# Kernel tuning notes

Hardware: AMD Instinct MI355X
Metric: run time of the kernel (lower is better)

The kernel has to match this reference:

```python
import jax, jax.numpy as jnp
import numpy as np

B, L, H, N, NL = 2, 160000, 128, 64, 4
TS, MR, CLS, LMAX = 1001, 16, 88, 1024
REP = TS * MR  # 16016


def setup_inputs() -> dict:
    key = jax.random.key(0)
    ks = jax.random.split(key, 16)
    def g(k, shape, s=0.02):
        return jax.random.normal(k, shape, jnp.float32) * s
    return {
        "x": jax.random.normal(ks[0], (B, L), jnp.float32),
        "enc_w": g(ks[1], (1, H), 1.0),
        "enc_b": g(ks[2], (H,)),
        "log_dt": jax.random.uniform(ks[3], (NL, H), jnp.float32, float(np.log(1e-3)), float(np.log(1e-1))),
        "log_A_real": jnp.log(0.5 * jnp.ones((NL, H, N), jnp.float32)),
        "A_imag": jnp.tile((np.pi * np.arange(N, dtype=np.float32))[None, None, :], (NL, H, 1)),
        "C_re": g(ks[4], (NL, H, N), 0.5 ** 0.5),
        "C_im": g(ks[5], (NL, H, N), 0.5 ** 0.5),
        "D": g(ks[6], (NL, H), 1.0),
        "out_w": g(ks[7], (NL, 2 * H, H), H ** -0.5),
        "out_b": g(ks[8], (NL, 2 * H)),
        "ln_g": jnp.ones((NL, H), jnp.float32),
        "ln_b": jnp.zeros((NL, H), jnp.float32),
        "dec_w": g(ks[9], (H, REP), H ** -0.5),
        "dec_b": g(ks[10], (REP,)),
        "head_w": g(ks[11], (4, MR, CLS), MR ** -0.5),
        "head_b": g(ks[12], (4, CLS)),
    }


def _s4_layer(u, log_dt, log_A_real, A_imag, C_re, C_im, D, out_w, out_b):
    # u: (B, H, L). S4D-style diagonal SSM kernel of length LMAX + FFT causal conv.
    dt = jnp.exp(log_dt)                         # (H,)
    A = -jnp.exp(log_A_real) + 1j * A_imag       # (H, N)
    C = C_re + 1j * C_im                         # (H, N)
    dtA = A * dt[:, None]                        # (H, N)
    Ct = C * (jnp.exp(dtA) - 1.0) / A            # ZOH-ish discretization
    l = jnp.arange(LMAX)
    vand = jnp.exp(dtA[:, :, None] * l)          # (H, N, LMAX) Vandermonde
    K = 2.0 * jnp.real(jnp.einsum('hn,hnl->hl', Ct, vand))  # (H, LMAX)
    n = L + LMAX                                 # linear (causal) conv via FFT
    uf = jnp.fft.rfft(u, n=n)                    # (B, H, n//2+1)
    kf = jnp.fft.rfft(K, n=n)                    # (H, n//2+1)
    y = jnp.fft.irfft(uf * kf[None], n=n)[..., :L]
    y = y + D[None, :, None] * u                 # skip connection
    y = jax.nn.gelu(y)
    # position-wise output linear H -> 2H, then GLU
    z = jnp.einsum('bhl,ph->bpl', y, out_w) + out_b[None, :, None]
    a, b = jnp.split(z, 2, axis=1)
    return a * jax.nn.sigmoid(b)


def _layernorm(v, g, b):
    # v: (B, L, H), normalize over H
    mu = v.mean(-1, keepdims=True)
    var = v.var(-1, keepdims=True)
    return (v - mu) / jnp.sqrt(var + 1e-5) * g + b


def reference(x, enc_w, enc_b, log_dt, log_A_real, A_imag, C_re, C_im, D,
              out_w, out_b, ln_g, ln_b, dec_w, dec_b, head_w, head_b):
    # encoder: (B, L, 1) -> (B, L, H)
    h = x[..., None] * enc_w[0][None, None, :] + enc_b  # (B, L, H)
    u = jnp.swapaxes(h, 1, 2)                            # (B, H, L)
    for i in range(NL):
        z = _s4_layer(u, log_dt[i], log_A_real[i], A_imag[i], C_re[i], C_im[i],
                      D[i], out_w[i], out_b[i])
        u = z + u                                        # residual
        v = _layernorm(jnp.swapaxes(u, 1, 2), ln_g[i], ln_b[i])  # post-norm
        u = jnp.swapaxes(v, 1, 2)
    feat = jnp.swapaxes(u, 1, 2).mean(axis=1)            # (B, H) mean-pool over L
    rep = feat @ dec_w + dec_b                           # (B, REP)
    rep = rep.reshape(B, TS, MR)                         # (B, 1001, 16)
    # 4 heads: [reg_onset, reg_offset, frame, velocity] stacked -> (4, B, TS, CLS)
    outs = jnp.einsum('btm,kmc->kbtc', rep, head_w) + head_b[:, None, None, :]
    return outs
```

## Files before the change

### kernel.cpp

```cpp
#include <hip/hip_runtime.h>
#include <math.h>

#define B_ 2
#define L_ 160000
#define H_ 128
#define N_ 64
#define NL_ 4
#define LMAX_ 1024
#define TS_ 1001
#define MR_ 16
#define CLS_ 88
#define REP_ 16016

#define NSUB_ 79
#define NJ_ 40
#define WIN_ 3208
#define WINS_ 3216
#define OUTB_ 2048
#define KE_STRIDE_ 1536
#define NST_ 10

typedef unsigned short ushort_t;
typedef unsigned int uint_t;
typedef short bf16x8 __attribute__((ext_vector_type(8)));
typedef float f32x4 __attribute__((ext_vector_type(4)));

__device__ __forceinline__ float bf2f(ushort_t h) {
  uint_t u = ((uint_t)h) << 16;
  return __uint_as_float(u);
}
__device__ __forceinline__ ushort_t f2bf(float f) {
  uint_t u = __float_as_uint(f);
  uint_t r = (u + 0x7fffu + ((u >> 16) & 1u)) >> 16;
  return (ushort_t)r;
}

__device__ __forceinline__ void lds_barrier() {
  asm volatile("s_waitcnt lgkmcnt(0)" ::: "memory");
  __builtin_amdgcn_sched_barrier(0);
  __builtin_amdgcn_s_barrier();
  __builtin_amdgcn_sched_barrier(0);
}

__global__ __launch_bounds__(256) void k_encode(const float* __restrict__ x,
                                                const float* __restrict__ enc_w,
                                                const float* __restrict__ enc_b,
                                                ushort_t* __restrict__ u) {
  int idx = blockIdx.x * 256 + threadIdx.x;
  int idx8 = idx * 8;
  int b = idx8 / (H_ * L_);
  int rem = idx8 - b * (H_ * L_);
  int h = rem / L_;
  int l = rem - h * L_;
  float w = enc_w[h], bb = enc_b[h];
  float4 x0 = *(const float4*)(x + b * L_ + l);
  float4 x1 = *(const float4*)(x + b * L_ + l + 4);
  union { ushort_t s[8]; uint4 v; } o;
  o.s[0] = f2bf(x0.x * w + bb); o.s[1] = f2bf(x0.y * w + bb);
  o.s[2] = f2bf(x0.z * w + bb); o.s[3] = f2bf(x0.w * w + bb);
  o.s[4] = f2bf(x1.x * w + bb); o.s[5] = f2bf(x1.y * w + bb);
  o.s[6] = f2bf(x1.z * w + bb); o.s[7] = f2bf(x1.w * w + bb);
  *(uint4*)(u + (size_t)(b * H_ + h) * L_ + l) = o.v;
}

__global__ __launch_bounds__(256) void k_ct(const float* __restrict__ log_dt,
                                            const float* __restrict__ log_A_real,
                                            const float* __restrict__ A_imag,
                                            const float* __restrict__ C_re,
                                            const float* __restrict__ C_im,
                                            float* __restrict__ ct,
                                            float* __restrict__ feat) {
  int idx = blockIdx.x * 256 + threadIdx.x;
  if (idx < B_ * H_) feat[idx] = 0.f;
  if (idx >= NL_ * H_ * N_) return;
  int h = (idx / N_) % H_;
  int i = idx / (N_ * H_);
  float dt = expf(log_dt[i * H_ + h]);
  float are = -expf(log_A_real[idx]);
  float aim = A_imag[idx];
  float dr = are * dt, di = aim * dt;
  float e = expf(dr);
  float si, co;
  sincosf(di, &si, &co);
  float er = e * co - 1.0f;
  float ei = e * si;
  float den = are * are + aim * aim;
  float qr = (er * are + ei * aim) / den;
  float qi = (ei * are - er * aim) / den;
  float cr = C_re[idx], cim = C_im[idx];
  double dd = (double)aim * (double)dt * 0.15915494309189535;
  dd -= floor(dd);
  uint_t P = (uint_t)(unsigned long long)(dd * 4294967296.0);
  ct[idx * 4 + 0] = dr;
  ct[idx * 4 + 1] = __uint_as_float(P);
  ct[idx * 4 + 2] = cr * qr - cim * qi;
  ct[idx * 4 + 3] = cr * qi + cim * qr;
}

__global__ __launch_bounds__(256) void k_ke(const float* __restrict__ ct,
                                            ushort_t* __restrict__ Ke) {
  int q = blockIdx.x & 3;
  int ih = blockIdx.x >> 2;
  __shared__ float4 cs[N_];
  if (threadIdx.x < N_) cs[threadIdx.x] = ((const float4*)ct)[ih * N_ + threadIdx.x];
  __syncthreads();
  for (int s = q * 384 + threadIdx.x; s < (q + 1) * 384; s += 256) {
    int d = s - 256;
    float val = 0.f;
    if (d >= 0 && d < LMAX_) {
      float fl = (float)d;
      float acc = 0.f;
      #pragma unroll 4
      for (int n = 0; n < N_; n++) {
        float4 qv = cs[n];
        float e = __expf(qv.x * fl);
        uint_t ph = __float_as_uint(qv.y) * (uint_t)d;
        float ang = (float)ph * 2.3283064365386963e-10f;
        float si = __builtin_amdgcn_sinf(ang);
        float co = __builtin_amdgcn_cosf(ang);
        acc += e * (qv.z * co - qv.w * si);
      }
      val = 2.f * acc;
    }
    Ke[(size_t)ih * KE_STRIDE_ + s] = f2bf(val);
  }
}

__global__ __launch_bounds__(256) void k_wprep(const float* __restrict__ W,
                                               ushort_t* __restrict__ Wb) {
  int idx = blockIdx.x * 256 + threadIdx.x;
  Wb[idx] = f2bf(W[idx]);
}

__global__ __launch_bounds__(256) void k_conv_mfma(const ushort_t* __restrict__ u,
                                                   const ushort_t* __restrict__ Ke,
                                                   const float* __restrict__ Dv,
                                                   ushort_t* __restrict__ y,
                                                   int layer) {
  int sub = blockIdx.x % NSUB_;
  int bh = blockIdx.x / NSUB_;
  int h = bh & (H_ - 1);
  int O0 = sub * OUTB_;
  int Gmax = O0 + 2063;
  __shared__ ushort_t win[4 * WINS_];
  __shared__ ushort_t kes[KE_STRIDE_];
  int tid = threadIdx.x;
  int lane = tid & 63, w = tid >> 6;
  int m = lane & 15, g = lane >> 4;

  {
    const ushort_t* keh0 = Ke + (size_t)(layer * H_ + h) * KE_STRIDE_;
    if (tid < KE_STRIDE_ / 8)
      *(bf16x8*)(kes + 8 * tid) = *(const bf16x8*)(keh0 + 8 * tid);
  }

  const ushort_t* ubh = u + (size_t)bh * L_;
  for (int T = tid; T < WIN_ / 8; T += 256) {
    int topt = Gmax - 8 * T;
    ushort_t vb[16];
    if (topt - 15 >= 0 && topt < L_) {
      union { uint4 q[2]; ushort_t s[16]; } ld;
      ld.q[0] = *(const uint4*)(ubh + topt - 15);
      ld.q[1] = *(const uint4*)(ubh + topt - 7);
      #pragma unroll
      for (int d = 0; d < 16; d++) vb[d] = ld.s[15 - d];
    } else {
      #pragma unroll
      for (int d = 0; d < 16; d++) {
        int gl = topt - d;
        vb[d] = (gl >= 0 && gl < L_) ? ubh[gl] : (ushort_t)0;
      }
    }
    #pragma unroll
    for (int p = 0; p < 4; p++) {
      union { bf16x8 v; ushort_t s[8]; } gr;
      #pragma unroll
      for (int e = 0; e < 8; e++) gr.s[e] = vb[p + e];
      *(bf16x8*)((char*)win + p * (2 * WINS_) + 16 * T) = gr.v;
    }
  }
  lds_barrier();

  const char* wb = (const char*)win;
  const ushort_t* kf0 = kes + 16 * m + 8 * g;
  int l0A = O0 + (w << 9);
  f32x4 accA = {0.f, 0.f, 0.f, 0.f}, accB = {0.f, 0.f, 0.f, 0.f};
  int t0 = Gmax - l0A - m + 8 * g - 256;
  bf16x8 ring[8];
  #pragma unroll
  for (int s = -8; s < NJ_; s++) {
    int tS = t0 + (s << 5);
    int pS = tS & 3;
    const char* base = wb + pS * (2 * WINS_) + 2 * (tS - pS);
    union { bf16x8 v; short4 h[2]; } f;
    f.h[0] = *(const short4*)base;
    f.h[1] = *(const short4*)(base + 8);
    if (s >= 0)
      accA = __builtin_amdgcn_mfma_f32_16x16x32_bf16(f.v, ring[s & 7], accA, 0, 0, 0);
    if (s <= 31) {
      bf16x8 kn = *(const bf16x8*)(kf0 + 32 * (s + 8));
      accB = __builtin_amdgcn_mfma_f32_16x16x32_bf16(f.v, kn, accB, 0, 0, 0);
      ring[(s + 8) & 7] = kn;
    }
  }

  float Dh = Dv[layer * H_ + h];
  ushort_t* ybh = y + (size_t)bh * L_;
  #pragma unroll
  for (int tile = 0; tile < 2; tile++) {
    f32x4 acc = tile ? accB : accA;
    int l0 = l0A + tile * 256;
    int outb = l0 + 16 * m + 4 * g;
    int tu = Gmax - outb - 3;
    int pu = tu & 3;
    union { short4 s4; ushort_t us[4]; } uu;
    uu.s4 = *(const short4*)(wb + pu * (2 * WINS_) + 2 * (tu - pu));
    union { ushort_t s[4]; short4 v; } pk;
    #pragma unroll
    for (int r = 0; r < 4; r++) {
      float uval = bf2f(uu.us[3 - r]);
      float v = acc[r] + Dh * uval;
      float z2 = 1.5957691216057308f * (v + 0.044715f * v * v * v);
      pk.s[r] = f2bf(v / (1.f + __expf(-z2)));
    }
    if (outb < L_) *(short4*)(ybh + outb) = pk.v;
  }
}

__global__ __launch_bounds__(256) void k_fused(const ushort_t* __restrict__ y,
                                               const ushort_t* __restrict__ Wb,
                                               const float* __restrict__ ob,
                                               ushort_t* __restrict__ u,
                                               const float* __restrict__ lng,
                                               const float* __restrict__ lnb,
                                               int last,
                                               float* __restrict__ feat) {
  __shared__ ushort_t yT[64 * 136];
  __shared__ float redS[4 * 64] __attribute__((aligned(16)));
  __shared__ float redQ[4 * 64] __attribute__((aligned(16)));
  __shared__ float redM[64] __attribute__((aligned(16)));
  __shared__ float redR[64] __attribute__((aligned(16)));
  int lblk = blockIdx.x, b = blockIdx.y;
  int tid = threadIdx.x;
  int lane = tid & 63, w = tid >> 6;
  int m = lane & 15, g = lane >> 4;
  int s = tid & 7, kkb = tid >> 3;
  int Lbase = lblk * (NST_ * 64);

  bf16x8 Wf[4][4];
  #pragma unroll
  for (int pj = 0; pj < 4; pj++) {
    int pbase = (pj < 2) ? (32 * w + 16 * pj) : (128 + 32 * w + 16 * (pj - 2));
    const ushort_t* wrow = Wb + (pbase + m) * 128 + 8 * g;
    #pragma unroll
    for (int ks = 0; ks < 4; ks++)
      Wf[pj][ks] = *(const bf16x8*)(wrow + 32 * ks);
  }
  float oba[2], obs[2], gam[2], bet[2];
  #pragma unroll
  for (int pj = 0; pj < 2; pj++) {
    int pa = 32 * w + 16 * pj + m;
    oba[pj] = ob[pa];
    obs[pj] = ob[pa + 128];
    gam[pj] = lng[pa];
    bet[pj] = lnb[pa];
  }

  uint4 sr[4];
  short4 un[2][4];
  #pragma unroll
  for (int p = 0; p < 4; p++)
    sr[p] = *(const uint4*)(y + ((size_t)b * H_ + kkb + 32 * p) * L_ + Lbase + 8 * s);
  #pragma unroll
  for (int pj = 0; pj < 2; pj++) {
    int pa = 32 * w + 16 * pj + m;
    const ushort_t* urow = u + (size_t)(b * H_ + pa) * L_ + Lbase;
    #pragma unroll
    for (int lj = 0; lj < 4; lj++)
      un[pj][lj] = *(const short4*)(urow + 16 * lj + 4 * g);
  }

  float poolAcc[2] = {0.f, 0.f};

  #pragma unroll
  for (int st = 0; st < NST_; st++) {
    int lc0 = Lbase + st * 64;

    uint4 srn[4];
    short4 unn[2][4];
    if (st < NST_ - 1) {
      int lc1 = lc0 + 64;
      #pragma unroll
      for (int p = 0; p < 4; p++)
        srn[p] = *(const uint4*)(y + ((size_t)b * H_ + kkb + 32 * p) * L_ + lc1 + 8 * s);
      #pragma unroll
      for (int pj = 0; pj < 2; pj++) {
        int pa = 32 * w + 16 * pj + m;
        const ushort_t* urow = u + (size_t)(b * H_ + pa) * L_ + lc1;
        #pragma unroll
        for (int lj = 0; lj < 4; lj++)
          unn[pj][lj] = *(const short4*)(urow + 16 * lj + 4 * g);
      }
    }

    #pragma unroll
    for (int p = 0; p < 4; p++) {
      int kk = kkb + 32 * p;
      const ushort_t* hp = (const ushort_t*)&sr[p];
      int sw = 8 * ((kk >> 3) ^ s) + (kk & 7);
      #pragma unroll
      for (int e = 0; e < 8; e++)
        yT[(8 * s + e) * 136 + sw] = hp[e];
    }
    lds_barrier();

    f32x4 acc[4][4];
    #pragma unroll
    for (int pj = 0; pj < 4; pj++)
      #pragma unroll
      for (int lj = 0; lj < 4; lj++) acc[pj][lj] = (f32x4){0.f, 0.f, 0.f, 0.f};
    #pragma unroll
    for (int ks = 0; ks < 4; ks++) {
      bf16x8 yf[4];
      #pragma unroll
      for (int lj = 0; lj < 4; lj++) {
        int l = 16 * lj + m;
        yf[lj] = *(const bf16x8*)(yT + l * 136 + 8 * ((4 * ks + g) ^ (l >> 3)));
      }
      #pragma unroll
      for (int pj = 0; pj < 4; pj++)
        #pragma unroll
        for (int lj = 0; lj < 4; lj++)
          acc[pj][lj] = __builtin_amdgcn_mfma_f32_16x16x32_bf16(yf[lj], Wf[pj][ks],
                                                                acc[pj][lj], 0, 0, 0);
    }

    #pragma unroll
    for (int pj = 0; pj < 2; pj++) {
      #pragma unroll
      for (int lj = 0; lj < 4; lj++) {
        #pragma unroll
        for (int r = 0; r < 4; r++) {
          float a = acc[pj][lj][r] + oba[pj];
          float sv = acc[pj + 2][lj][r] + obs[pj];
          float uor = bf2f(((const ushort_t*)&un[pj][lj])[r]);
          acc[pj][lj][r] = a * (1.f / (1.f + __expf(-sv))) + uor;
        }
      }
    }

    #pragma unroll
    for (int lj = 0; lj < 4; lj++) {
      #pragma unroll
      for (int r = 0; r < 4; r++) {
        float v0 = acc[0][lj][r], v1 = acc[1][lj][r];
        float sm = v0 + v1, q = v0 * v0 + v1 * v1;
        sm += __shfl_xor(sm, 1);  q += __shfl_xor(q, 1);
        sm += __shfl_xor(sm, 2);  q += __shfl_xor(q, 2);
        sm += __shfl_xor(sm, 4);  q += __shfl_xor(q, 4);
        sm += __shfl_xor(sm, 8);  q += __shfl_xor(q, 8);
        if (m == 0) {
          int l = 16 * lj + 4 * g + r;
          redS[w * 64 + l] = sm;
          redQ[w * 64 + l] = q;
        }
      }
    }
    lds_barrier();
    if (tid < 64) {
      float sm = redS[tid] + redS[64 + tid] + redS[128 + tid] + redS[192 + tid];
      float q = redQ[tid] + redQ[64 + tid] + redQ[128 + tid] + redQ[192 + tid];
      float mean = sm * (1.f / 128.f);
      float var = q * (1.f / 128.f) - mean * mean;
      redM[tid] = mean;
      redR[tid] = rsqrtf(var + 1e-5f);
    }
    lds_barrier();

    #pragma unroll
    for (int pj = 0; pj < 2; pj++) {
      int pa = 32 * w + 16 * pj + m;
      ushort_t* urow = u + (size_t)(b * H_ + pa) * L_ + lc0;
      #pragma unroll
      for (int lj = 0; lj < 4; lj++) {
        int l0 = 16 * lj + 4 * g;
        f32x4 mn = *(const f32x4*)(redM + l0);
        f32x4 rs = *(const f32x4*)(redR + l0);
        if (!last) {
          union { ushort_t sx[4]; short4 v; } pk;
          #pragma unroll
          for (int r = 0; r < 4; r++)
            pk.sx[r] = f2bf((acc[pj][lj][r] - mn[r]) * rs[r] * gam[pj] + bet[pj]);
          *(short4*)(urow + l0) = pk.v;
        } else {
          #pragma unroll
          for (int r = 0; r < 4; r++)
            poolAcc[pj] += (acc[pj][lj][r] - mn[r]) * rs[r] * gam[pj] + bet[pj];
        }
      }
    }

    #pragma unroll
    for (int p = 0; p < 4; p++) sr[p] = srn[p];
    #pragma unroll
    for (int pj = 0; pj < 2; pj++)
      #pragma unroll
      for (int lj = 0; lj < 4; lj++) un[pj][lj] = unn[pj][lj];
  }

  if (last) {
    #pragma unroll
    for (int pj = 0; pj < 2; pj++) {
      int pa = 32 * w + 16 * pj + m;
      float pool = poolAcc[pj];
      pool += __shfl_xor(pool, 16);
      pool += __shfl_xor(pool, 32);
      if (g == 0) atomicAdd(&feat[b * H_ + pa], pool * (1.f / L_));
    }
  }
}

__global__ __launch_bounds__(256) void k_dec(const float* __restrict__ feat,
                                             const float* __restrict__ dw,
                                             const float* __restrict__ db,
                                             float* __restrict__ rep) {
  int idx = blockIdx.x * 256 + threadIdx.x;
  if (idx >= B_ * REP_) return;
  int b = idx / REP_, r = idx - b * REP_;
  float s = db[r];
  #pragma unroll 8
  for (int h = 0; h < H_; h++) s = fmaf(feat[b * H_ + h], dw[h * REP_ + r], s);
  rep[idx] = s;
}

__global__ __launch_bounds__(256) void k_head(const float* __restrict__ rep,
                                              const float* __restrict__ hw,
                                              const float* __restrict__ hb,
                                              float* __restrict__ out) {
  int idx = blockIdx.x * 256 + threadIdx.x;
  if (idx >= 4 * B_ * TS_ * CLS_) return;
  int c = idx % CLS_;
  int t = (idx / CLS_) % TS_;
  int b = (idx / (CLS_ * TS_)) % B_;
  int k = idx / (CLS_ * TS_ * B_);
  float s = hb[k * CLS_ + c];
  const float* rp = rep + ((long long)b * TS_ + t) * MR_;
  #pragma unroll
  for (int m = 0; m < MR_; m++) s = fmaf(rp[m], hw[(k * MR_ + m) * CLS_ + c], s);
  out[idx] = s;
}

extern "C" void kernel_launch(void* const* d_in, const int* in_sizes, int n_in,
                              void* d_out, int out_size, void* d_ws, size_t ws_size,
                              hipStream_t stream) {
  const float* x = (const float*)d_in[0];
  const float* enc_w = (const float*)d_in[1];
  const float* enc_b = (const float*)d_in[2];
  const float* log_dt = (const float*)d_in[3];
  const float* log_A_real = (const float*)d_in[4];
  const float* A_imag = (const float*)d_in[5];
  const float* C_re = (const float*)d_in[6];
  const float* C_im = (const float*)d_in[7];
  const float* Dv = (const float*)d_in[8];
  const float* out_w = (const float*)d_in[9];
  const float* out_b = (const float*)d_in[10];
  const float* ln_g = (const float*)d_in[11];
  const float* ln_b = (const float*)d_in[12];
  const float* dec_w = (const float*)d_in[13];
  const float* dec_b = (const float*)d_in[14];
  const float* head_w = (const float*)d_in[15];
  const float* head_b = (const float*)d_in[16];

  if (ws_size < 167000000ULL) return;

  float* ws = (float*)d_ws;
  ushort_t* u = (ushort_t*)ws;
  ushort_t* y = (ushort_t*)(ws + 20480000);
  ushort_t* Ke = (ushort_t*)(ws + 20480000 + 20480000);
  float* ct = ws + 20480000 + 20480000 + 393216;
  ushort_t* Wb = (ushort_t*)(ct + 131072);
  float* feat = ct + 131072 + 65536;
  float* rep = feat + 256;

  k_encode<<<(B_ * H_ * L_ / 8 + 255) / 256, 256, 0, stream>>>(x, enc_w, enc_b, u);
  k_ct<<<(NL_ * H_ * N_ + 255) / 256, 256, 0, stream>>>(log_dt, log_A_real, A_imag,
                                                        C_re, C_im, ct, feat);
  k_ke<<<NL_ * H_ * 4, 256, 0, stream>>>(ct, Ke);
  k_wprep<<<NL_ * 256 * 128 / 256, 256, 0, stream>>>(out_w, Wb);

  for (int i = 0; i < NL_; i++) {
    k_conv_mfma<<<B_ * H_ * NSUB_, 256, 0, stream>>>(u, Ke, Dv, y, i);
    k_fused<<<dim3(L_ / (NST_ * 64), B_), 256, 0, stream>>>(
        y, Wb + (size_t)i * 256 * 128, out_b + i * 256, u,
        ln_g + i * H_, ln_b + i * H_, (i == NL_ - 1) ? 1 : 0, feat);
  }
  k_dec<<<(B_ * REP_ + 255) / 256, 256, 0, stream>>>(feat, dec_w, dec_b, rep);
  k_head<<<(4 * B_ * TS_ * CLS_ + 255) / 256, 256, 0, stream>>>(rep, head_w, head_b,
                                                               (float*)d_out);
}
```

Before: 994.7 us.

## Store activations in blocked (B, L/64, H, 64) layout to contiguize fused-kernel tiles

```diff
diff --git a/kernel.cpp b/kernel.cpp
--- a/kernel.cpp
+++ b/kernel.cpp
@@ -12,13 +12,15 @@
 #define CLS_ 88
 #define REP_ 16016
 
+#define NB_ 2500
+#define HB_ 8192
 #define NSUB_ 79
 #define NJ_ 40
 #define WIN_ 3208
 #define WINS_ 3216
 #define OUTB_ 2048
 #define KE_STRIDE_ 1536
-#define NST_ 10
+#define NSTF_ 4
 
 typedef unsigned short ushort_t;
 typedef unsigned int uint_t;
@@ -60,7 +62,8 @@
   o.s[2] = f2bf(x0.z * w + bb); o.s[3] = f2bf(x0.w * w + bb);
   o.s[4] = f2bf(x1.x * w + bb); o.s[5] = f2bf(x1.y * w + bb);
   o.s[6] = f2bf(x1.z * w + bb); o.s[7] = f2bf(x1.w * w + bb);
-  *(uint4*)(u + (size_t)(b * H_ + h) * L_ + l) = o.v;
+  size_t addr = ((size_t)b * NB_ + (l >> 6)) * HB_ + h * 64 + (l & 63);
+  *(uint4*)(u + addr) = o.v;
 }
 
 __global__ __launch_bounds__(256) void k_ct(const float* __restrict__ log_dt,
@@ -140,6 +143,7 @@
   int sub = blockIdx.x % NSUB_;
   int bh = blockIdx.x / NSUB_;
   int h = bh & (H_ - 1);
+  int b = bh >> 7;
   int O0 = sub * OUTB_;
   int Gmax = O0 + 2063;
   __shared__ ushort_t win[4 * WINS_];
@@ -154,23 +158,28 @@
       *(bf16x8*)(kes + 8 * tid) = *(const bf16x8*)(keh0 + 8 * tid);
   }
 
-  const ushort_t* ubh = u + (size_t)bh * L_;
+  const ushort_t* UB = u + (size_t)b * NB_ * HB_ + h * 64;
   for (int T = tid; T < WIN_ / 8; T += 256) {
     int topt = Gmax - 8 * T;
+    ushort_t tmp[16];
+    #pragma unroll
+    for (int half = 0; half < 2; half++) {
+      int x = topt - 15 + 8 * half;
+      if (x >= 0 && x + 7 < L_) {
+        *(uint4*)&tmp[8 * half] =
+            *(const uint4*)(UB + (size_t)(x >> 6) * HB_ + (x & 63));
+      } else {
+        #pragma unroll
+        for (int j = 0; j < 8; j++) {
+          int gl = x + j;
+          tmp[8 * half + j] = (gl >= 0 && gl < L_)
+              ? UB[(size_t)(gl >> 6) * HB_ + (gl & 63)] : (ushort_t)0;
+        }
+      }
+    }
     ushort_t vb[16];
-    if (topt - 15 >= 0 && topt < L_) {
-      union { uint4 q[2]; ushort_t s[16]; } ld;
-      ld.q[0] = *(const uint4*)(ubh + topt - 15);
-      ld.q[1] = *(const uint4*)(ubh + topt - 7);
-      #pragma unroll
-      for (int d = 0; d < 16; d++) vb[d] = ld.s[15 - d];
-    } else {
-      #pragma unroll
-      for (int d = 0; d < 16; d++) {
-        int gl = topt - d;
-        vb[d] = (gl >= 0 && gl < L_) ? ubh[gl] : (ushort_t)0;
-      }
-    }
+    #pragma unroll
+    for (int d = 0; d < 16; d++) vb[d] = tmp[15 - d];
     #pragma unroll
     for (int p = 0; p < 4; p++) {
       union { bf16x8 v; ushort_t s[8]; } gr;
@@ -205,7 +214,7 @@
   }
 
   float Dh = Dv[layer * H_ + h];
-  ushort_t* ybh = y + (size_t)bh * L_;
+  ushort_t* YB = y + (size_t)b * NB_ * HB_ + h * 64;
   #pragma unroll
   for (int tile = 0; tile < 2; tile++) {
     f32x4 acc = tile ? accB : accA;
@@ -223,7 +232,8 @@
       float z2 = 1.5957691216057308f * (v + 0.044715f * v * v * v);
       pk.s[r] = f2bf(v / (1.f + __expf(-z2)));
     }
-    if (outb < L_) *(short4*)(ybh + outb) = pk.v;
+    if (outb < L_)
+      *(short4*)(YB + (size_t)(outb >> 6) * HB_ + (outb & 63)) = pk.v;
   }
 }
 
@@ -245,7 +255,7 @@
   int lane = tid & 63, w = tid >> 6;
   int m = lane & 15, g = lane >> 4;
   int s = tid & 7, kkb = tid >> 3;
-  int Lbase = lblk * (NST_ * 64);
+  int nb0 = lblk * NSTF_;
 
   bf16x8 Wf[4][4];
   #pragma unroll
@@ -266,40 +276,46 @@
     bet[pj] = lnb[pa];
   }
 
+  const ushort_t* ybase = y + (size_t)b * NB_ * HB_;
+  ushort_t* ubase = u + (size_t)b * NB_ * HB_;
+
   uint4 sr[4];
   short4 un[2][4];
+  {
+    const ushort_t* yb = ybase + (size_t)nb0 * HB_;
+    #pragma unroll
+    for (int p = 0; p < 4; p++)
+      sr[p] = *(const uint4*)(yb + (kkb + 32 * p) * 64 + 8 * s);
+    const ushort_t* ub = ubase + (size_t)nb0 * HB_;
+    #pragma unroll
+    for (int pj = 0; pj < 2; pj++) {
+      int pa = 32 * w + 16 * pj + m;
+      #pragma unroll
+      for (int lj = 0; lj < 4; lj++)
+        un[pj][lj] = *(const short4*)(ub + pa * 64 + 16 * lj + 4 * g);
+    }
+  }
+
+  float poolAcc[2] = {0.f, 0.f};
+
   #pragma unroll
-  for (int p = 0; p < 4; p++)
-    sr[p] = *(const uint4*)(y + ((size_t)b * H_ + kkb + 32 * p) * L_ + Lbase + 8 * s);
-  #pragma unroll
-  for (int pj = 0; pj < 2; pj++) {
-    int pa = 32 * w + 16 * pj + m;
-    const ushort_t* urow = u + (size_t)(b * H_ + pa) * L_ + Lbase;
-    #pragma unroll
-    for (int lj = 0; lj < 4; lj++)
-      un[pj][lj] = *(const short4*)(urow + 16 * lj + 4 * g);
-  }
-
-  float poolAcc[2] = {0.f, 0.f};
-
-  #pragma unroll
-  for (int st = 0; st < NST_; st++) {
-    int lc0 = Lbase + st * 64;
+  for (int st = 0; st < NSTF_; st++) {
+    int nb = nb0 + st;
 
     uint4 srn[4];
     short4 unn[2][4];
-    if (st < NST_ - 1) {
-      int lc1 = lc0 + 64;
+    if (st < NSTF_ - 1) {
+      const ushort_t* yb = ybase + (size_t)(nb + 1) * HB_;
       #pragma unroll
       for (int p = 0; p < 4; p++)
-        srn[p] = *(const uint4*)(y + ((size_t)b * H_ + kkb + 32 * p) * L_ + lc1 + 8 * s);
+        srn[p] = *(const uint4*)(yb + (kkb + 32 * p) * 64 + 8 * s);
+      const ushort_t* ub = ubase + (size_t)(nb + 1) * HB_;
       #pragma unroll
       for (int pj = 0; pj < 2; pj++) {
         int pa = 32 * w + 16 * pj + m;
-        const ushort_t* urow = u + (size_t)(b * H_ + pa) * L_ + lc1;
         #pragma unroll
         for (int lj = 0; lj < 4; lj++)
-          unn[pj][lj] = *(const short4*)(urow + 16 * lj + 4 * g);
+          unn[pj][lj] = *(const short4*)(ub + pa * 64 + 16 * lj + 4 * g);
       }
     }
 
@@ -377,10 +393,10 @@
     }
     lds_barrier();
 
+    ushort_t* ub = ubase + (size_t)nb * HB_;
     #pragma unroll
     for (int pj = 0; pj < 2; pj++) {
       int pa = 32 * w + 16 * pj + m;
-      ushort_t* urow = u + (size_t)(b * H_ + pa) * L_ + lc0;
       #pragma unroll
       for (int lj = 0; lj < 4; lj++) {
         int l0 = 16 * lj + 4 * g;
@@ -391,7 +407,7 @@
           #pragma unroll
           for (int r = 0; r < 4; r++)
             pk.sx[r] = f2bf((acc[pj][lj][r] - mn[r]) * rs[r] * gam[pj] + bet[pj]);
-          *(short4*)(urow + l0) = pk.v;
+          *(short4*)(ub + pa * 64 + l0) = pk.v;
         } else {
           #pragma unroll
           for (int r = 0; r < 4; r++)
@@ -490,7 +506,7 @@
 
   for (int i = 0; i < NL_; i++) {
     k_conv_mfma<<<B_ * H_ * NSUB_, 256, 0, stream>>>(u, Ke, Dv, y, i);
-    k_fused<<<dim3(L_ / (NST_ * 64), B_), 256, 0, stream>>>(
+    k_fused<<<dim3(NB_ / NSTF_, B_), 256, 0, stream>>>(
         y, Wb + (size_t)i * 256 * 128, out_b + i * 256, u,
         ln_g + i * H_, ln_b + i * H_, (i == NL_ - 1) ? 1 : 0, feat);
   }
```

Measured after the change: 1.031 ms. 1.04x slower.
